# Optimization experiments

Measured on AMD Instinct MI355X. Metric: run time of the kernel, lower is better.

## Reference

```python
import jax, jax.numpy as jnp
import numpy as np

NUM_HEADS = 4
HEAD_DIM = 16  # out_channels // num_heads = 64 // 4
IN_C = 64
OUT_C = 64


def setup_inputs() -> dict:
    key = jax.random.key(0)
    k1, k2, k3 = jax.random.split(key, 3)
    x = jax.random.normal(k1, (2, IN_C, 64, 64), dtype=jnp.float32)
    # nn.Linear(in_channels, 3*out_channels): weight (3*OUT_C, IN_C), bias (3*OUT_C,)
    s = 1.0 / np.sqrt(IN_C)
    qkv_w = jax.random.uniform(k2, (3 * OUT_C, IN_C), minval=-s, maxval=s, dtype=jnp.float32)
    qkv_b = jax.random.uniform(k3, (3 * OUT_C,), minval=-s, maxval=s, dtype=jnp.float32)
    return {"x": x, "qkv_w": qkv_w, "qkv_b": qkv_b}


def reference(x, qkv_w, qkv_b):
    B, C, H, W = x.shape
    N = H * W
    # (B,C,H,W) -> (B,N,C)
    tokens = x.reshape(B, C, N).transpose(0, 2, 1)
    qkv = tokens @ qkv_w.T + qkv_b  # (B,N,3*OUT_C)
    q, k, v = jnp.split(qkv, 3, axis=-1)
    def to_heads(t):
        return t.reshape(B, N, NUM_HEADS, HEAD_DIM).transpose(0, 2, 1, 3)  # (B,h,N,d)
    q, k, v = to_heads(q), to_heads(k), to_heads(v)
    scale = 1.0 / np.sqrt(HEAD_DIM)
    attn = jnp.einsum('bhnd,bhmd->bhnm', q, k) * scale  # (B,h,N,N)
    attn = jax.nn.softmax(attn, axis=-1)
    # dropout is identity in eval mode
    out = jnp.einsum('bhnm,bhmd->bhnd', attn, v)  # (B,h,N,d)
    out = out.transpose(0, 2, 1, 3).reshape(B, N, OUT_C)  # (B,N,outC)
    out = out.transpose(0, 2, 1).reshape(B, OUT_C, H, W)
    return out
```

## Files before the change

kernel.cpp:

```cpp
#include <hip/hip_runtime.h>
#include <hip/hip_bf16.h>


#define NTOK 4096
#define HD   16
#define BH   8
#define KT   128
#define SCH  (KT/16)
#define HALFK 2048
#define NSTAGE (HALFK/KT)

typedef __attribute__((ext_vector_type(4))) short short4v;
typedef __attribute__((ext_vector_type(4))) float float4v;
typedef __attribute__((ext_vector_type(4))) ushort ushort4v;
typedef __attribute__((ext_vector_type(2))) unsigned uint2v;

__device__ __forceinline__ ushort f2bf(float f) {
  unsigned u = __builtin_bit_cast(unsigned, f);
  u += 0x7fffu + ((u >> 16) & 1u);
  return (ushort)(u >> 16);
}

__device__ __forceinline__ float fast_exp2(float x) {
#if __has_builtin(__builtin_amdgcn_exp2f)
  return __builtin_amdgcn_exp2f(x);
#else
  return exp2f(x);
#endif
}

__device__ __forceinline__ short4v pack4_bf16(float a, float b, float c, float d) {
  __hip_bfloat162 lo = __float22bfloat162_rn(make_float2(a, b));
  __hip_bfloat162 hi = __float22bfloat162_rn(make_float2(c, d));
  unsigned ulo, uhi;
  __builtin_memcpy(&ulo, &lo, 4);
  __builtin_memcpy(&uhi, &hi, 4);
  uint2v u = { ulo, uhi };
  return __builtin_bit_cast(short4v, u);
}

#define QB_OFF 0
#define KB_OFF ((size_t)BH*NTOK*HD)
#define VT_OFF (2*(size_t)BH*NTOK*HD)

__global__ __launch_bounds__(192) void qkv_proj(
    const float* __restrict__ x, const float* __restrict__ w,
    const float* __restrict__ bias, ushort* __restrict__ wsu) {
  const int TOK = 8, TILES = 2;
  int blk = blockIdx.x;
  int b   = blk >> 8;
  int n00 = (blk & 255) * (TOK*TILES);
  int o   = threadIdx.x;

  float wr[64];
  const float4* w4 = reinterpret_cast<const float4*>(w + o*64);
  #pragma unroll
  for (int i = 0; i < 16; ++i) {
    float4 tt = w4[i];
    wr[4*i+0]=tt.x; wr[4*i+1]=tt.y; wr[4*i+2]=tt.z; wr[4*i+3]=tt.w;
  }
  float bb = bias[o];

  int part = o >> 6;
  int oo   = o & 63;
  int h    = oo >> 4;
  int dd   = oo & 15;
  int bh   = b*4 + h;
  const float QSCALE = 0.25f * 1.44269504f;

  ushort* Qt = wsu + QB_OFF;
  ushort* Kb = wsu + KB_OFF;
  ushort* Vt = wsu + VT_OFF;

  __shared__ float4 xs4[64][2];
  const float4* x4 = reinterpret_cast<const float4*>(x);

  #pragma unroll 1
  for (int tile = 0; tile < TILES; ++tile) {
    int n0 = n00 + tile*TOK;
    for (int idx = threadIdx.x; idx < 128; idx += 192) {
      int c = idx >> 1, t4 = idx & 1;
      xs4[c][t4] = x4[((size_t)b*64 + c)*(NTOK/4) + (n0 >> 2) + t4];
    }
    __syncthreads();

    #pragma unroll
    for (int t4 = 0; t4 < 2; ++t4) {
      float a[4] = {bb, bb, bb, bb};
      #pragma unroll
      for (int c = 0; c < 64; ++c) {
        float4 xv = xs4[c][t4];
        float wv = wr[c];
        a[0] = fmaf(xv.x, wv, a[0]);
        a[1] = fmaf(xv.y, wv, a[1]);
        a[2] = fmaf(xv.z, wv, a[2]);
        a[3] = fmaf(xv.w, wv, a[3]);
      }
      if (part == 0) {
        ushort4v vv = { f2bf(a[0]*QSCALE), f2bf(a[1]*QSCALE),
                        f2bf(a[2]*QSCALE), f2bf(a[3]*QSCALE) };
        *(ushort4v*)(Qt + ((size_t)bh*HD + dd)*NTOK + n0 + t4*4) = vv;
      } else if (part == 1) {
        #pragma unroll
        for (int j = 0; j < 4; ++j)
          Kb[((size_t)bh*NTOK + n0 + t4*4 + j)*HD + dd] = f2bf(a[j]);
      } else {
        ushort4v vv = { f2bf(a[0]), f2bf(a[1]), f2bf(a[2]), f2bf(a[3]) };
        *(ushort4v*)(Vt + ((size_t)bh*HD + dd)*NTOK + n0 + t4*4) = vv;
      }
    }
    __syncthreads();
  }
}

__global__ __launch_bounds__(256, 4) void attn_mfma(
    const ushort* __restrict__ wsu, float* __restrict__ out) {
  const ushort* Qt = wsu + QB_OFF;
  const ushort* Kb = wsu + KB_OFF;
  const ushort* Vt = wsu + VT_OFF;

  int bh   = blockIdx.x >> 7;
  int qblk = blockIdx.x & 127;
  int tid  = threadIdx.x;
  int wid  = tid >> 6;
  int lane = tid & 63;
  int lr   = lane & 15;
  int g4   = (lane >> 4) << 2;
  int qg   = wid & 1;
  int half = wid >> 1;
  int qbase = qblk*32 + qg*16;

  __shared__ __align__(16) char tiles[2][2][2][4096];
  __shared__ float comb[2][64][5];

  const ushort* Qh = Qt + (size_t)bh*NTOK*HD;
  const ushort* Kh = Kb + (size_t)bh*NTOK*HD + (size_t)half*HALFK*HD;
  const ushort* Vh = Vt + (size_t)bh*HD*NTOK + half*HALFK;

  short4v qf;
  qf[0] = (short)Qh[(size_t)(g4+0)*NTOK + qbase + lr];
  qf[1] = (short)Qh[(size_t)(g4+1)*NTOK + qbase + lr];
  qf[2] = (short)Qh[(size_t)(g4+2)*NTOK + qbase + lr];
  qf[3] = (short)Qh[(size_t)(g4+3)*NTOK + qbase + lr];

  size_t kgoff = (size_t)((lane >> 5)*16 + (lane & 15))*HD + ((lane >> 4) & 1)*8;
  size_t vgoff = (size_t)(lane & 15)*NTOK + (lane >> 4)*8;

  int loff = ((lane >> 5) << 8) + ((lane & 15) << 4) + (((lane >> 4) & 1) << 3);

  const short4v one4 = {(short)0x3F80, (short)0x3F80, (short)0x3F80, (short)0x3F80};

  float4v acc_e = {0.f,0.f,0.f,0.f}, acc_o = {0.f,0.f,0.f,0.f};
  float4v lac_e = {0.f,0.f,0.f,0.f}, lac_o = {0.f,0.f,0.f,0.f};

#define GLL(g, l_) __builtin_amdgcn_global_load_lds(                        \
    (const __attribute__((address_space(1))) unsigned*)(g),                 \
    (__attribute__((address_space(3))) unsigned*)(l_), 16, 0, 0)

#define STAGE(buf, s) do {                                                  \
    if (qg == 0) {                                                          \
      const ushort* gs = Kh + (size_t)(s)*(KT*HD) + kgoff;                  \
      char* lb = &tiles[buf][half][0][0];                                   \
      GLL(gs, lb); GLL(gs+512, lb+1024);                                    \
      GLL(gs+1024, lb+2048); GLL(gs+1536, lb+3072);                         \
    } else {                                                                \
      const ushort* gs = Vh + (size_t)(s)*KT + vgoff;                       \
      char* lb = &tiles[buf][half][1][0];                                   \
      GLL(gs, lb); GLL(gs+32, lb+1024);                                     \
      GLL(gs+64, lb+2048); GLL(gs+96, lb+3072);                             \
    } } while (0)

#define COMPUTE(buf) do {                                                   \
    const char* kb = &tiles[buf][half][0][0];                               \
    const char* vb = &tiles[buf][half][1][0];                               \
    __builtin_amdgcn_s_setprio(1);                                          \
    _Pragma("unroll")                                                       \
    for (int p = 0; p < SCH/2; ++p) {                                       \
      short4v kf_e = *(const short4v*)(kb + p*1024       + loff);           \
      short4v kf_o = *(const short4v*)(kb + p*1024 + 512 + loff);           \
      short4v vf_e = *(const short4v*)(vb + p*1024       + loff);           \
      short4v vf_o = *(const short4v*)(vb + p*1024 + 512 + loff);           \
      float4v zero = {0.f,0.f,0.f,0.f};                                     \
      float4v se = __builtin_amdgcn_mfma_f32_16x16x16bf16_1k(kf_e, qf, zero, 0,0,0); \
      float4v so = __builtin_amdgcn_mfma_f32_16x16x16bf16_1k(kf_o, qf, zero, 0,0,0); \
      float pe0 = fast_exp2(se[0]), pe1 = fast_exp2(se[1]);                 \
      float pe2 = fast_exp2(se[2]), pe3 = fast_exp2(se[3]);                 \
      float po0 = fast_exp2(so[0]), po1 = fast_exp2(so[1]);                 \
      float po2 = fast_exp2(so[2]), po3 = fast_exp2(so[3]);                 \
      short4v pbe = pack4_bf16(pe0, pe1, pe2, pe3);                         \
      short4v pbo = pack4_bf16(po0, po1, po2, po3);                         \
      acc_e = __builtin_amdgcn_mfma_f32_16x16x16bf16_1k(vf_e, pbe, acc_e, 0,0,0); \
      acc_o = __builtin_amdgcn_mfma_f32_16x16x16bf16_1k(vf_o, pbo, acc_o, 0,0,0); \
      lac_e = __builtin_amdgcn_mfma_f32_16x16x16bf16_1k(one4, pbe, lac_e, 0,0,0); \
      lac_o = __builtin_amdgcn_mfma_f32_16x16x16bf16_1k(one4, pbo, lac_o, 0,0,0); \
    }                                                                       \
    __builtin_amdgcn_s_setprio(0);                                          \
    } while (0)

  STAGE(0, 0);
  __syncthreads();

  #pragma unroll 1
  for (int s = 0; s < NSTAGE; s += 2) {
    if (s + 1 < NSTAGE) STAGE(1, s + 1);
    COMPUTE(0);
    __syncthreads();
    if (s + 2 < NSTAGE) STAGE(0, s + 2);
    COMPUTE(1);
    __syncthreads();
  }

  float a0 = acc_e[0] + acc_o[0];
  float a1 = acc_e[1] + acc_o[1];
  float a2 = acc_e[2] + acc_o[2];
  float a3 = acc_e[3] + acc_o[3];
  float ls = lac_e[0] + lac_o[0];

  if (half == 1) {
    comb[qg][lane][0] = a0; comb[qg][lane][1] = a1;
    comb[qg][lane][2] = a2; comb[qg][lane][3] = a3;
    comb[qg][lane][4] = ls;
  }
  __syncthreads();
  if (half == 0) {
    a0 += comb[qg][lane][0]; a1 += comb[qg][lane][1];
    a2 += comb[qg][lane][2]; a3 += comb[qg][lane][3];
    ls += comb[qg][lane][4];
    float inv = 1.0f / ls;
    int b = bh >> 2, h = bh & 3;
    float* ob = out + ((size_t)(b*64 + h*16 + g4)) * NTOK;
    ob[           qbase + lr] = a0 * inv;
    ob[  NTOK   + qbase + lr] = a1 * inv;
    ob[2*NTOK   + qbase + lr] = a2 * inv;
    ob[3*NTOK   + qbase + lr] = a3 * inv;
  }
#undef GLL
#undef STAGE
#undef COMPUTE
}

extern "C" void kernel_launch(void* const* d_in, const int* in_sizes, int n_in,
                              void* d_out, int out_size, void* d_ws, size_t ws_size,
                              hipStream_t stream) {
  const float* x    = (const float*)d_in[0];
  const float* w    = (const float*)d_in[1];
  const float* bias = (const float*)d_in[2];
  float* out  = (float*)d_out;
  ushort* wsu = (ushort*)d_ws;

  qkv_proj <<<512,  192, 0, stream>>>(x, w, bias, wsu);
  attn_mfma<<<1024, 256, 0, stream>>>(wsu, out);
}
```

Baseline: 43.23 us.

## Split keys into four wave quarters with direct register loads and shared K/V fragments

The attention kernel drops LDS staging through global_load_lds with double buffering. Each of the four waves now handles a quarter of the key range for all 32 queries of the block, loading K/V fragments straight from global memory into registers with one-iteration prefetch. Each K/V fragment is reused for two query tiles, and the row sum is accumulated with scalar adds instead of extra MFMAs against a ones vector. The cost is more global/L2 traffic per wave with no LDS sharing, more register pressure, and a wider three-way cross-wave reduction at the end.

```diff
diff --git a/kernel.cpp b/kernel.cpp
--- a/kernel.cpp
+++ b/kernel.cpp
@@ -5,10 +5,8 @@
 #define NTOK 4096
 #define HD   16
 #define BH   8
-#define KT   128
-#define SCH  (KT/16)
-#define HALFK 2048
-#define NSTAGE (HALFK/KT)
+#define QUART 1024
+#define PITERS (QUART/32)
 
 typedef __attribute__((ext_vector_type(4))) short short4v;
 typedef __attribute__((ext_vector_type(4))) float float4v;
@@ -119,124 +117,116 @@
   const ushort* Kb = wsu + KB_OFF;
   const ushort* Vt = wsu + VT_OFF;
 
-  int bh   = blockIdx.x >> 7;
-  int qblk = blockIdx.x & 127;
-  int tid  = threadIdx.x;
-  int wid  = tid >> 6;
-  int lane = tid & 63;
-  int lr   = lane & 15;
-  int g4   = (lane >> 4) << 2;
-  int qg   = wid & 1;
-  int half = wid >> 1;
-  int qbase = qblk*32 + qg*16;
-
-  __shared__ __align__(16) char tiles[2][2][2][4096];
-  __shared__ float comb[2][64][5];
-
-  const ushort* Qh = Qt + (size_t)bh*NTOK*HD;
-  const ushort* Kh = Kb + (size_t)bh*NTOK*HD + (size_t)half*HALFK*HD;
-  const ushort* Vh = Vt + (size_t)bh*HD*NTOK + half*HALFK;
-
-  short4v qf;
-  qf[0] = (short)Qh[(size_t)(g4+0)*NTOK + qbase + lr];
-  qf[1] = (short)Qh[(size_t)(g4+1)*NTOK + qbase + lr];
-  qf[2] = (short)Qh[(size_t)(g4+2)*NTOK + qbase + lr];
-  qf[3] = (short)Qh[(size_t)(g4+3)*NTOK + qbase + lr];
-
-  size_t kgoff = (size_t)((lane >> 5)*16 + (lane & 15))*HD + ((lane >> 4) & 1)*8;
-  size_t vgoff = (size_t)(lane & 15)*NTOK + (lane >> 4)*8;
-
-  int loff = ((lane >> 5) << 8) + ((lane & 15) << 4) + (((lane >> 4) & 1) << 3);
-
-  const short4v one4 = {(short)0x3F80, (short)0x3F80, (short)0x3F80, (short)0x3F80};
-
-  float4v acc_e = {0.f,0.f,0.f,0.f}, acc_o = {0.f,0.f,0.f,0.f};
-  float4v lac_e = {0.f,0.f,0.f,0.f}, lac_o = {0.f,0.f,0.f,0.f};
-
-#define GLL(g, l_) __builtin_amdgcn_global_load_lds(                        \
-    (const __attribute__((address_space(1))) unsigned*)(g),                 \
-    (__attribute__((address_space(3))) unsigned*)(l_), 16, 0, 0)
-
-#define STAGE(buf, s) do {                                                  \
-    if (qg == 0) {                                                          \
-      const ushort* gs = Kh + (size_t)(s)*(KT*HD) + kgoff;                  \
-      char* lb = &tiles[buf][half][0][0];                                   \
-      GLL(gs, lb); GLL(gs+512, lb+1024);                                    \
-      GLL(gs+1024, lb+2048); GLL(gs+1536, lb+3072);                         \
-    } else {                                                                \
-      const ushort* gs = Vh + (size_t)(s)*KT + vgoff;                       \
-      char* lb = &tiles[buf][half][1][0];                                   \
-      GLL(gs, lb); GLL(gs+32, lb+1024);                                     \
-      GLL(gs+64, lb+2048); GLL(gs+96, lb+3072);                             \
-    } } while (0)
-
-#define COMPUTE(buf) do {                                                   \
-    const char* kb = &tiles[buf][half][0][0];                               \
-    const char* vb = &tiles[buf][half][1][0];                               \
-    __builtin_amdgcn_s_setprio(1);                                          \
-    _Pragma("unroll")                                                       \
-    for (int p = 0; p < SCH/2; ++p) {                                       \
-      short4v kf_e = *(const short4v*)(kb + p*1024       + loff);           \
-      short4v kf_o = *(const short4v*)(kb + p*1024 + 512 + loff);           \
-      short4v vf_e = *(const short4v*)(vb + p*1024       + loff);           \
-      short4v vf_o = *(const short4v*)(vb + p*1024 + 512 + loff);           \
-      float4v zero = {0.f,0.f,0.f,0.f};                                     \
-      float4v se = __builtin_amdgcn_mfma_f32_16x16x16bf16_1k(kf_e, qf, zero, 0,0,0); \
-      float4v so = __builtin_amdgcn_mfma_f32_16x16x16bf16_1k(kf_o, qf, zero, 0,0,0); \
-      float pe0 = fast_exp2(se[0]), pe1 = fast_exp2(se[1]);                 \
-      float pe2 = fast_exp2(se[2]), pe3 = fast_exp2(se[3]);                 \
-      float po0 = fast_exp2(so[0]), po1 = fast_exp2(so[1]);                 \
-      float po2 = fast_exp2(so[2]), po3 = fast_exp2(so[3]);                 \
-      short4v pbe = pack4_bf16(pe0, pe1, pe2, pe3);                         \
-      short4v pbo = pack4_bf16(po0, po1, po2, po3);                         \
-      acc_e = __builtin_amdgcn_mfma_f32_16x16x16bf16_1k(vf_e, pbe, acc_e, 0,0,0); \
-      acc_o = __builtin_amdgcn_mfma_f32_16x16x16bf16_1k(vf_o, pbo, acc_o, 0,0,0); \
-      lac_e = __builtin_amdgcn_mfma_f32_16x16x16bf16_1k(one4, pbe, lac_e, 0,0,0); \
-      lac_o = __builtin_amdgcn_mfma_f32_16x16x16bf16_1k(one4, pbo, lac_o, 0,0,0); \
-    }                                                                       \
-    __builtin_amdgcn_s_setprio(0);                                          \
-    } while (0)
-
-  STAGE(0, 0);
+  int bh    = blockIdx.x >> 7;
+  int qblk  = blockIdx.x & 127;
+  int tid   = threadIdx.x;
+  int quart = tid >> 6;
+  int lane  = tid & 63;
+  int lr    = lane & 15;
+  int g4    = (lane >> 4) << 2;
+  int qbase = qblk*32;
+
+  __shared__ float comb[3][64][11];
+
+  const ushort* Qh = Qt + (size_t)bh*HD*NTOK;
+  const ushort* Kh = Kb + ((size_t)bh*NTOK + (size_t)quart*QUART)*HD;
+  const ushort* Vh = Vt + (size_t)bh*HD*NTOK + quart*QUART;
+
+  short4v qf0, qf1;
+  #pragma unroll
+  for (int j = 0; j < 4; ++j) {
+    qf0[j] = (short)Qh[(size_t)(g4+j)*NTOK + qbase      + lr];
+    qf1[j] = (short)Qh[(size_t)(g4+j)*NTOK + qbase + 16 + lr];
+  }
+
+  const ushort* kp = Kh + lr*HD + (lane >> 4)*4;
+  const ushort* vp = Vh + (size_t)lr*NTOK + (lane >> 4)*4;
+
+  float4v a0e = {0.f,0.f,0.f,0.f}, a0o = {0.f,0.f,0.f,0.f};
+  float4v a1e = {0.f,0.f,0.f,0.f}, a1o = {0.f,0.f,0.f,0.f};
+  float l0 = 0.f, l1 = 0.f;
+
+  short4v kfe = *(const short4v*)(kp);
+  short4v kfo = *(const short4v*)(kp + 256);
+  short4v vfe = *(const short4v*)(vp);
+  short4v vfo = *(const short4v*)(vp + 16);
+
+  #pragma unroll 2
+  for (int it = 0; it < PITERS; ++it) {
+    short4v nkfe, nkfo, nvfe, nvfo;
+    if (it + 1 < PITERS) {
+      nkfe = *(const short4v*)(kp + (it+1)*512);
+      nkfo = *(const short4v*)(kp + (it+1)*512 + 256);
+      nvfe = *(const short4v*)(vp + (it+1)*32);
+      nvfo = *(const short4v*)(vp + (it+1)*32 + 16);
+    }
+    float4v zero = {0.f,0.f,0.f,0.f};
+    __builtin_amdgcn_s_setprio(1);
+    float4v s0e = __builtin_amdgcn_mfma_f32_16x16x16bf16_1k(kfe, qf0, zero, 0,0,0);
+    float4v s0o = __builtin_amdgcn_mfma_f32_16x16x16bf16_1k(kfo, qf0, zero, 0,0,0);
+    float4v s1e = __builtin_amdgcn_mfma_f32_16x16x16bf16_1k(kfe, qf1, zero, 0,0,0);
+    float4v s1o = __builtin_amdgcn_mfma_f32_16x16x16bf16_1k(kfo, qf1, zero, 0,0,0);
+
+    float p0e0 = fast_exp2(s0e[0]), p0e1 = fast_exp2(s0e[1]);
+    float p0e2 = fast_exp2(s0e[2]), p0e3 = fast_exp2(s0e[3]);
+    float p0o0 = fast_exp2(s0o[0]), p0o1 = fast_exp2(s0o[1]);
+    float p0o2 = fast_exp2(s0o[2]), p0o3 = fast_exp2(s0o[3]);
+    float p1e0 = fast_exp2(s1e[0]), p1e1 = fast_exp2(s1e[1]);
+    float p1e2 = fast_exp2(s1e[2]), p1e3 = fast_exp2(s1e[3]);
+    float p1o0 = fast_exp2(s1o[0]), p1o1 = fast_exp2(s1o[1]);
+    float p1o2 = fast_exp2(s1o[2]), p1o3 = fast_exp2(s1o[3]);
+
+    l0 += (p0e0 + p0e1) + (p0e2 + p0e3) + (p0o0 + p0o1) + (p0o2 + p0o3);
+    l1 += (p1e0 + p1e1) + (p1e2 + p1e3) + (p1o0 + p1o1) + (p1o2 + p1o3);
+
+    short4v pb0e = pack4_bf16(p0e0, p0e1, p0e2, p0e3);
+    short4v pb0o = pack4_bf16(p0o0, p0o1, p0o2, p0o3);
+    short4v pb1e = pack4_bf16(p1e0, p1e1, p1e2, p1e3);
+    short4v pb1o = pack4_bf16(p1o0, p1o1, p1o2, p1o3);
+
+    a0e = __builtin_amdgcn_mfma_f32_16x16x16bf16_1k(vfe, pb0e, a0e, 0,0,0);
+    a0o = __builtin_amdgcn_mfma_f32_16x16x16bf16_1k(vfo, pb0o, a0o, 0,0,0);
+    a1e = __builtin_amdgcn_mfma_f32_16x16x16bf16_1k(vfe, pb1e, a1e, 0,0,0);
+    a1o = __builtin_amdgcn_mfma_f32_16x16x16bf16_1k(vfo, pb1o, a1o, 0,0,0);
+    __builtin_amdgcn_s_setprio(0);
+
+    kfe = nkfe; kfo = nkfo; vfe = nvfe; vfo = nvfo;
+  }
+
+  float o0[4], o1[4];
+  #pragma unroll
+  for (int r = 0; r < 4; ++r) {
+    o0[r] = a0e[r] + a0o[r];
+    o1[r] = a1e[r] + a1o[r];
+  }
+
+  if (quart != 0) {
+    float* cp = &comb[quart-1][lane][0];
+    cp[0] = o0[0]; cp[1] = o0[1]; cp[2] = o0[2]; cp[3] = o0[3];
+    cp[4] = o1[0]; cp[5] = o1[1]; cp[6] = o1[2]; cp[7] = o1[3];
+    cp[8] = l0;    cp[9] = l1;
+  }
   __syncthreads();
-
-  #pragma unroll 1
-  for (int s = 0; s < NSTAGE; s += 2) {
-    if (s + 1 < NSTAGE) STAGE(1, s + 1);
-    COMPUTE(0);
-    __syncthreads();
-    if (s + 2 < NSTAGE) STAGE(0, s + 2);
-    COMPUTE(1);
-    __syncthreads();
-  }
-
-  float a0 = acc_e[0] + acc_o[0];
-  float a1 = acc_e[1] + acc_o[1];
-  float a2 = acc_e[2] + acc_o[2];
-  float a3 = acc_e[3] + acc_o[3];
-  float ls = lac_e[0] + lac_o[0];
-
-  if (half == 1) {
-    comb[qg][lane][0] = a0; comb[qg][lane][1] = a1;
-    comb[qg][lane][2] = a2; comb[qg][lane][3] = a3;
-    comb[qg][lane][4] = ls;
-  }
-  __syncthreads();
-  if (half == 0) {
-    a0 += comb[qg][lane][0]; a1 += comb[qg][lane][1];
-    a2 += comb[qg][lane][2]; a3 += comb[qg][lane][3];
-    ls += comb[qg][lane][4];
-    float inv = 1.0f / ls;
+  if (quart == 0) {
+    #pragma unroll
+    for (int wv = 0; wv < 3; ++wv) {
+      const float* cp = &comb[wv][lane][0];
+      o0[0] += cp[0]; o0[1] += cp[1]; o0[2] += cp[2]; o0[3] += cp[3];
+      o1[0] += cp[4]; o1[1] += cp[5]; o1[2] += cp[6]; o1[3] += cp[7];
+      l0 += cp[8];    l1 += cp[9];
+    }
+    l0 += __shfl_xor(l0, 16); l0 += __shfl_xor(l0, 32);
+    l1 += __shfl_xor(l1, 16); l1 += __shfl_xor(l1, 32);
+    float inv0 = 1.0f / l0, inv1 = 1.0f / l1;
+
     int b = bh >> 2, h = bh & 3;
     float* ob = out + ((size_t)(b*64 + h*16 + g4)) * NTOK;
-    ob[           qbase + lr] = a0 * inv;
-    ob[  NTOK   + qbase + lr] = a1 * inv;
-    ob[2*NTOK   + qbase + lr] = a2 * inv;
-    ob[3*NTOK   + qbase + lr] = a3 * inv;
-  }
-#undef GLL
-#undef STAGE
-#undef COMPUTE
+    #pragma unroll
+    for (int r = 0; r < 4; ++r) {
+      ob[(size_t)r*NTOK + qbase      + lr] = o0[r] * inv0;
+      ob[(size_t)r*NTOK + qbase + 16 + lr] = o1[r] * inv1;
+    }
+  }
 }
 
 extern "C" void kernel_launch(void* const* d_in, const int* in_sizes, int n_in,
```

Result: slower. 55.33 us (+28.0%).
